# Performance work log

Measured on AMD Instinct MI355X. Metric: run time of the kernel, lower is better.

## Reference

```python
import jax, jax.numpy as jnp
import numpy as np
from functools import partial

U, I, D, E = 8192, 8192, 128, 524288
N = U + I


def setup_inputs() -> dict:
    key = jax.random.key(0)
    ks = jax.random.split(key, 12)
    s = 1.0 / np.sqrt(D)
    return {
        "user_emb": jax.random.normal(ks[0], (U, D), jnp.float32) * 0.1,
        "item_emb": jax.random.normal(ks[1], (I, D), jnp.float32) * 0.1,
        "adj_rows": jax.random.randint(ks[2], (E,), 0, N, jnp.int32),
        "adj_cols": jax.random.randint(ks[3], (E,), 0, N, jnp.int32),
        "adj_vals": jax.random.uniform(ks[4], (E,), jnp.float32) * (1.0 / 32.0),
        "wq": jax.random.normal(ks[5], (D, D), jnp.float32) * s,
        "bq": jnp.zeros((D,), jnp.float32),
        "wk": jax.random.normal(ks[6], (D, D), jnp.float32) * s,
        "bk": jnp.zeros((D,), jnp.float32),
        "wv": jax.random.normal(ks[7], (D, D), jnp.float32) * s,
        "bv": jnp.zeros((D,), jnp.float32),
        "fw": jax.random.normal(ks[8], (D, D), jnp.float32) * s,
        "fb": jnp.zeros((D,), jnp.float32),
        "n_layers": 3,
        "topk": 32,
    }


def _spmm(vals, rows, cols, x):
    # sparse [N,N] @ dense [N,D] via gather + segment_sum
    return jax.ops.segment_sum(vals[:, None] * x[cols], rows, num_segments=N)


def reference(user_emb, item_emb, adj_rows, adj_cols, adj_vals,
              wq, bq, wk, bk, wv, bv, fw, fb, n_layers, topk):
    ego = jnp.concatenate([user_emb, item_emb], axis=0)  # [N, D]
    layers = []
    for _ in range(n_layers):
        ego = _spmm(adj_vals, adj_rows, adj_cols, ego)
        layers.append(ego)
    all_emb = jnp.mean(jnp.stack(layers, axis=1), axis=1)  # [N, D]

    # full similarity + topk + gather
    sim = ego @ ego.T                                # [N, N]
    idx = jax.lax.top_k(sim, topk)[1]                # [N, K]
    samples = jnp.take(ego, idx, axis=0)             # [N, K, D]

    # per-node small attention over the K samples (dropout = eval identity)
    q = ego @ wq.T + bq                              # [N, D]
    k_ = samples @ wk.T + bk                         # [N, K, D]
    v = samples @ wv.T + bv                          # [N, K, D]
    scores = jnp.einsum('nd,nkd->nk', q, k_) / jnp.sqrt(jnp.float32(D))
    attn = jax.nn.softmax(scores, axis=-1)
    atten_embed = jnp.einsum('nk,nkd->nd', attn, v) + 0.1 * ego

    # fusion gating (softmax over dim=1, i.e. the node axis, as in source)
    a1 = jnp.tanh(all_emb @ fw.T + fb)
    a2 = jnp.tanh(atten_embed @ fw.T + fb)
    a = jax.nn.softmax(jnp.stack([a1, a2], axis=0), axis=1)  # [2, N, D]
    fusion = a[0] * all_emb + a[1] * atten_embed

    return (all_emb[:U], all_emb[U:],
            atten_embed[:U], atten_embed[U:],
            fusion[:U], fusion[U:])
```

## Files before the change

### kernel.cpp

```cpp
#include <hip/hip_runtime.h>
#include <math.h>

#define U_ 8192
#define I_ 8192
#define D_ 128
#define E_ 524288
#define N_ 16384
#define K_ 32
#define CAP_ 512

typedef unsigned short u16;
typedef unsigned int u32;
typedef unsigned long long u64;
typedef __attribute__((ext_vector_type(8))) short bf16x8;
typedef __attribute__((ext_vector_type(4))) float f32x4;

__global__ void k_init(const float* __restrict__ wq, const float* __restrict__ wk,
                       const float* __restrict__ bq, const float* __restrict__ wv,
                       const float* __restrict__ fw,
                       float* __restrict__ M, float* __restrict__ bqk,
                       float* __restrict__ wvT, float* __restrict__ fwdT,
                       int* __restrict__ cnt, float* __restrict__ cs1,
                       float* __restrict__ cs2,
                       float* __restrict__ svec, int* __restrict__ gcount,
                       int* __restrict__ failn) {
  const int tid = blockIdx.x * 256 + threadIdx.x;
  cnt[tid] = 0;
  gcount[tid] = 0;
  if (tid < 2048) { cs1[tid] = 0.f; cs2[tid] = 0.f; }
  if (tid < 128) svec[tid] = 0.f;
  if (tid == 0) *failn = 0;
  const int i = tid >> 7, j = tid & 127;
  float s = 0.f;
  for (int l = 0; l < 128; ++l) s += wq[l * 128 + i] * wk[l * 128 + j];
  M[tid] = s;
  wvT[i * 128 + j] = wv[j * 128 + i];
  fwdT[i * 128 + j] = fw[j * 128 + i];
  if (tid < 128) {
    float s2 = 0.f;
    for (int l = 0; l < 128; ++l) s2 += bq[l] * wk[l * 128 + tid];
    bqk[tid] = s2;
  }
}

__global__ void k_concat(const float* __restrict__ user, const float* __restrict__ item,
                         float* __restrict__ ego) {
  const int i = blockIdx.x * 256 + threadIdx.x;
  ego[i] = (i < U_ * D_) ? user[i] : item[i - U_ * D_];
}

__global__ void k_hist(const int* __restrict__ rows, int* __restrict__ cnt) {
  const int e = blockIdx.x * 256 + threadIdx.x;
  atomicAdd(&cnt[rows[e]], 1);
}

__global__ void k_scan(const int* __restrict__ cnt, int* __restrict__ row_ptr,
                       int* __restrict__ cursor) {
  __shared__ int wsum[16];
  __shared__ int carry_s;
  const int t = threadIdx.x;
  const int lane = t & 63, wid = t >> 6;
  if (t == 0) carry_s = 0;
  __syncthreads();
  for (int c = 0; c < N_ / 1024; ++c) {
    const int x = cnt[c * 1024 + t];
    int incl = x;
#pragma unroll
    for (int off = 1; off < 64; off <<= 1) {
      const int v = __shfl_up(incl, off, 64);
      if (lane >= off) incl += v;
    }
    if (lane == 63) wsum[wid] = incl;
    __syncthreads();
    if (wid == 0) {
      int s = (lane < 16) ? wsum[lane] : 0;
#pragma unroll
      for (int off = 1; off < 16; off <<= 1) {
        const int v = __shfl_up(s, off, 64);
        if (lane >= off) s += v;
      }
      if (lane < 16) wsum[lane] = s;
    }
    __syncthreads();
    const int carry = carry_s;
    const int wbase = wid ? wsum[wid - 1] : 0;
    const int excl = carry + wbase + incl - x;
    row_ptr[c * 1024 + t] = excl;
    cursor[c * 1024 + t] = excl;
    __syncthreads();
    if (t == 1023) carry_s += wsum[15];
    __syncthreads();
  }
  if (t == 0) row_ptr[N_] = carry_s;
}

__global__ void k_scatter(const int* __restrict__ rows, const int* __restrict__ cols,
                          const float* __restrict__ vals, int* __restrict__ cursor,
                          int* __restrict__ ccol, float* __restrict__ cval) {
  const int e = blockIdx.x * 256 + threadIdx.x;
  const int r = rows[e];
  const int p = atomicAdd(&cursor[r], 1);
  ccol[p] = cols[e];
  cval[p] = vals[e];
}

__global__ __launch_bounds__(128) void k_spmm(const float* __restrict__ x,
                                              float* __restrict__ y,
                                              float* __restrict__ sum,
                                              const int* __restrict__ row_ptr,
                                              const int* __restrict__ ccol,
                                              const float* __restrict__ cval,
                                              const int first) {
  const int r = blockIdx.x, d = threadIdx.x;
  const int b = row_ptr[r], e = row_ptr[r + 1];
  double acc = 0.0;
  for (int i = b; i < e; ++i)
    acc += (double)cval[i] * (double)x[ccol[i] * 128 + d];
  const float f = (float)acc;
  y[r * 128 + d] = f;
  if (first) sum[r * 128 + d] = f; else sum[r * 128 + d] += f;
}

__global__ void k_div3(float* __restrict__ a) {
  const int i = blockIdx.x * 256 + threadIdx.x;
  a[i] = a[i] / 3.0f;
}

__global__ __launch_bounds__(256) void k_split_t(const float* __restrict__ x,
                                                 u16* __restrict__ Gh, u16* __restrict__ Gl,
                                                 u16* __restrict__ XTh, u16* __restrict__ XTl,
                                                 float* __restrict__ svec) {
  __shared__ u16 lh[128 * 66];
  __shared__ u16 ll[128 * 66];
  const int tid = threadIdx.x;
  const int r0 = blockIdx.x * 64;
  float colsum = 0.f;
  for (int s = 0; s < 32; ++s) {
    const int idx = tid + s * 256;
    const int r = idx >> 7, d = idx & 127;
    const float v = x[(r0 + r) * 128 + d];
    colsum += v;
    unsigned int u = __float_as_uint(v);
    u += 0x7fffu + ((u >> 16) & 1u);
    const u16 h = (u16)(u >> 16);
    const float hf = __uint_as_float(((unsigned int)h) << 16);
    const float l = v - hf;
    unsigned int u2 = __float_as_uint(l);
    u2 += 0x7fffu + ((u2 >> 16) & 1u);
    const u16 lo = (u16)(u2 >> 16);
    Gh[(r0 + r) * 128 + d] = h;
    Gl[(r0 + r) * 128 + d] = lo;
    lh[d * 66 + r] = h;
    ll[d * 66 + r] = lo;
  }
  atomicAdd(&svec[tid & 127], colsum);
  __syncthreads();
  for (int s = 0; s < 32; ++s) {
    const int idx = tid + s * 256;
    const int d = idx >> 6, rr = idx & 63;
    XTh[d * 16384 + r0 + rr] = lh[d * 66 + rr];
    XTl[d * 16384 + r0 + rr] = ll[d * 66 + rr];
  }
}

__global__ __launch_bounds__(256) void k_c2mfma(const u16* __restrict__ XTh,
                                                const u16* __restrict__ XTl,
                                                float* __restrict__ C2part) {
  const int tid = threadIdx.x, w = tid >> 6, lane = tid & 63;
  const int n16 = lane & 15, kq = lane >> 4;
  const int c0 = blockIdx.x * 64;
  f32x4 acc[2][8];
#pragma unroll
  for (int a = 0; a < 2; ++a)
#pragma unroll
    for (int b = 0; b < 8; ++b) acc[a][b] = (f32x4){0.f, 0.f, 0.f, 0.f};
  for (int ks = 0; ks < 2; ++ks) {
    const int c = c0 + ks * 32 + kq * 8;
    bf16x8 Fh[8], Fl[8];
#pragma unroll
    for (int g = 0; g < 8; ++g) {
      const int base = (g * 16 + n16) * 16384 + c;
      Fh[g] = *(const bf16x8*)&XTh[base];
      Fl[g] = *(const bf16x8*)&XTl[base];
    }
#pragma unroll
    for (int a = 0; a < 2; ++a) {
      const int tr = w * 2 + a;
#pragma unroll
      for (int b = 0; b < 8; ++b) {
        acc[a][b] = __builtin_amdgcn_mfma_f32_16x16x32_bf16(Fl[tr], Fh[b], acc[a][b], 0, 0, 0);
        acc[a][b] = __builtin_amdgcn_mfma_f32_16x16x32_bf16(Fh[tr], Fl[b], acc[a][b], 0, 0, 0);
        acc[a][b] = __builtin_amdgcn_mfma_f32_16x16x32_bf16(Fh[tr], Fh[b], acc[a][b], 0, 0, 0);
      }
    }
  }
  float* dst = C2part + (size_t)blockIdx.x * 16384;
#pragma unroll
  for (int a = 0; a < 2; ++a) {
    const int tr = w * 2 + a;
#pragma unroll
    for (int b = 0; b < 8; ++b)
#pragma unroll
      for (int i = 0; i < 4; ++i)
        dst[(tr * 16 + kq * 4 + i) * 128 + b * 16 + n16] = acc[a][b][i];
  }
}

__global__ void k_c2red(const float* __restrict__ C2part, float* __restrict__ C2) {
  const int e = blockIdx.x * 256 + threadIdx.x;
  float s = 0.f;
  for (int b = 0; b < 256; ++b) s += C2part[(size_t)b * 16384 + e];
  C2[e] = s;
}

__global__ __launch_bounds__(128) void k_tau(const float* __restrict__ x,
                                             const float* __restrict__ C2,
                                             const float* __restrict__ svec,
                                             float* __restrict__ tau) {
  __shared__ float xs[128];
  __shared__ double red[128];
  const int n = blockIdx.x, tid = threadIdx.x;
  xs[tid] = x[n * 128 + tid];
  __syncthreads();
  double y = 0.0;
  for (int k2 = 0; k2 < 128; ++k2) y += (double)xs[k2] * (double)C2[k2 * 128 + tid];
  red[tid] = (double)xs[tid] * y;
  __syncthreads();
  for (int s = 64; s; s >>= 1) { if (tid < s) red[tid] += red[tid + s]; __syncthreads(); }
  const double exy = red[0] / 16384.0;
  __syncthreads();
  red[tid] = (double)xs[tid] * (double)svec[tid];
  __syncthreads();
  for (int s = 64; s; s >>= 1) { if (tid < s) red[tid] += red[tid + s]; __syncthreads(); }
  if (tid == 0) {
    const double m = red[0] / 16384.0;
    double var = exy - m * m;
    if (var < 0.0) var = 0.0;
    tau[n] = (float)(m + 2.55 * sqrt(var));
  }
}

__global__ __launch_bounds__(256) void k_qk(const float* __restrict__ ego,
                                            const float* __restrict__ M,
                                            const float* __restrict__ bqk,
                                            float* __restrict__ qkout) {
  __shared__ float xs[8][128];
  const int tid = threadIdx.x;
  const int r0 = blockIdx.x * 8;
#pragma unroll
  for (int s = 0; s < 4; ++s) {
    const int idx = tid + s * 256;
    xs[idx >> 7][idx & 127] = ego[r0 * 128 + idx];
  }
  __syncthreads();
  const int j = tid & 127, h = tid >> 7;
  const float bj = bqk[j];
  float acc[4];
#pragma unroll
  for (int r = 0; r < 4; ++r) acc[r] = bj;
  for (int d = 0; d < 128; d += 4) {
    const float w0 = M[(d + 0) * 128 + j];
    const float w1 = M[(d + 1) * 128 + j];
    const float w2 = M[(d + 2) * 128 + j];
    const float w3 = M[(d + 3) * 128 + j];
#pragma unroll
    for (int r = 0; r < 4; ++r) {
      const float4 xv = *(const float4*)&xs[h * 4 + r][d];
      acc[r] += xv.x * w0 + xv.y * w1 + xv.z * w2 + xv.w * w3;
    }
  }
#pragma unroll
  for (int r = 0; r < 4; ++r)
    qkout[(r0 + h * 4 + r) * 128 + j] = acc[r];
}

__device__ __forceinline__ void gload_lds16(const u16* g, u16* l) {
  __builtin_amdgcn_global_load_lds(
      (const __attribute__((address_space(1))) void*)g,
      (__attribute__((address_space(3))) void*)l, 16, 0, 0);
}

__global__ __launch_bounds__(256) void k_simmfma(const u16* __restrict__ Gh,
                                                 const u16* __restrict__ Gl,
                                                 const float* __restrict__ tau,
                                                 int* __restrict__ gstripcnt,
                                                 int2* __restrict__ gbuf) {
  __shared__ __align__(16) u16 lh[64 * 128];
  __shared__ int cnt128[128];
  const int tid = threadIdx.x;
  const int w = tid >> 6, lane = tid & 63;
  const int strip = blockIdx.x & 15, rgrp = blockIdx.x >> 4;
  const int n16 = lane & 15, kq = lane >> 4;

  if (tid < 128) cnt128[tid] = 0;

  const int rowbase = rgrp * 128 + w * 32;
  bf16x8 Bh[2][4], Bl[2][4];
#pragma unroll
  for (int rg = 0; rg < 2; ++rg) {
    const int row = rowbase + rg * 16 + n16;
#pragma unroll
    for (int q = 0; q < 4; ++q) {
      Bh[rg][q] = *(const bf16x8*)&Gh[row * 128 + q * 32 + kq * 8];
      Bl[rg][q] = *(const bf16x8*)&Gl[row * 128 + q * 32 + kq * 8];
    }
  }
  const float tau0 = tau[rowbase + n16];
  const float tau1 = tau[rowbase + 16 + n16];
  const int col0 = strip * 1024;

  for (int st = 0; st < 16; ++st) {
    const int cb = col0 + st * 64;
    __syncthreads();
#pragma unroll
    for (int ii = 0; ii < 4; ++ii) {
      const int srow = w * 16 + ii * 4 + kq;
      const int chunk = n16 ^ (srow & 7);
      gload_lds16(Gh + (((size_t)(cb + srow)) << 7) + chunk * 8,
                  lh + ((w * 16 + ii * 4) << 7));
    }
    __syncthreads();
#pragma unroll
    for (int ct = 0; ct < 4; ++ct) {
      const int ar = ct * 16 + n16;
      const char* lbase = (const char*)lh + ar * 256;
      bf16x8 Ah[4];
#pragma unroll
      for (int q = 0; q < 4; ++q)
        Ah[q] = *(const bf16x8*)(lbase + ((q * 64 + kq * 16) ^ ((ar & 7) << 4)));
#pragma unroll
      for (int rg = 0; rg < 2; ++rg) {
        f32x4 p = {0.f, 0.f, 0.f, 0.f};
        f32x4 r = {0.f, 0.f, 0.f, 0.f};
#pragma unroll
        for (int q = 0; q < 4; ++q) {
          p = __builtin_amdgcn_mfma_f32_16x16x32_bf16(Ah[q], Bh[rg][q], p, 0, 0, 0);
          r = __builtin_amdgcn_mfma_f32_16x16x32_bf16(Ah[q], Bl[rg][q], r, 0, 0, 0);
        }
        const float tv = rg ? tau1 : tau0;
        const int lrow = w * 32 + rg * 16 + n16;
        const int row = rgrp * 128 + lrow;
#pragma unroll
        for (int i = 0; i < 4; ++i) {
          const float v = p[i] + r[i];
          if (v > tv) {
            const int c = cb + ct * 16 + kq * 4 + i;
            const int pos = atomicAdd(&cnt128[lrow], 1);
            if (pos < 32)
              gbuf[row * CAP_ + strip * 32 + pos] = make_int2(c, __float_as_int(v));
          }
        }
      }
    }
  }
  __syncthreads();
  if (tid < 128) gstripcnt[(rgrp * 128 + tid) * 16 + strip] = cnt128[tid];
}

__global__ void k_check(const int* __restrict__ gstripcnt, int* __restrict__ failq,
                        int* __restrict__ failn) {
  const int n = blockIdx.x * 256 + threadIdx.x;
  int total = 0; int over = 0;
#pragma unroll
  for (int s = 0; s < 16; ++s) {
    const int c = gstripcnt[n * 16 + s];
    total += c;
    over |= (c > 32);
  }
  if (total < 36 || total > CAP_ || over) {
    const int s = atomicAdd(failn, 1);
    if (s < 64) failq[s] = n;
  }
}

__global__ __launch_bounds__(256) void k_refine(const int* __restrict__ gstripcnt,
                                                const int2* __restrict__ gbuf,
                                                int* __restrict__ topk_idx) {
  __shared__ u64 lk[4][CAP_];
  const int tid = threadIdx.x, w = tid >> 6, lane = tid & 63;
  const int n = blockIdx.x * 4 + w;

  const int scn = (lane < 16) ? gstripcnt[n * 16 + lane] : 0;
  int total = 0, over = 0;
#pragma unroll
  for (int s = 0; s < 16; ++s) {
    const int c = __shfl(scn, s, 64);
    total += c;
    over |= (c > 32);
  }
  const int bad = (total < 36 || total > CAP_ || over);
  const int cnt = bad ? 0 : total;

  int base = 0;
#pragma unroll
  for (int s = 0; s < 16; ++s) {
    const int c = __shfl(scn, s, 64);
    if (!bad && lane < c) {
      const int2 p = gbuf[n * CAP_ + s * 32 + lane];
      u32 uv = (u32)p.y;
      uv = (uv >> 31) ? ~uv : (uv | 0x80000000u);
      lk[w][base + lane] = ((u64)uv << 32) | (u64)(16383 - p.x);
    }
    base += bad ? 0 : c;
  }
  __syncthreads();

  for (int ci = lane; ci < cnt; ci += 64) {
    const u64 kk = lk[w][ci];
    int r = 0;
#pragma unroll 4
    for (int j = 0; j < cnt; ++j)
      r += (lk[w][j] > kk) ? 1 : 0;
    if (r < 32) topk_idx[n * 32 + r] = 16383 - (int)(u32)(kk & 0xffffffffu);
  }
  if (bad && lane < 32) topk_idx[n * 32 + lane] = 0;
}

__global__ __launch_bounds__(256) void k_fallback(const float* __restrict__ x,
                                                  const int* __restrict__ failq,
                                                  const int* __restrict__ failn,
                                                  double* __restrict__ fsim,
                                                  int* __restrict__ topk_idx) {
  const int nf = *failn;
  const int which = blockIdx.x;
  if (which >= nf || which >= 64) return;
  const int row = failq[which];
  __shared__ float xs[128];
  __shared__ double bm[256];
  __shared__ int bc[256];
  const int tid = threadIdx.x;
  if (tid < 128) xs[tid] = x[row * 128 + tid];
  __syncthreads();
  double* fs = fsim + (size_t)which * 16384;
  for (int c = tid; c < 16384; c += 256) {
    const float4* xp = (const float4*)&x[c * 128];
    double a = 0.0;
    for (int d = 0; d < 32; ++d) {
      const float4 v = xp[d];
      a += (double)xs[d * 4 + 0] * (double)v.x + (double)xs[d * 4 + 1] * (double)v.y +
           (double)xs[d * 4 + 2] * (double)v.z + (double)xs[d * 4 + 3] * (double)v.w;
    }
    fs[c] = a;
  }
  __syncthreads();
  for (int r = 0; r < 32; ++r) {
    double m = -1.0e300; int mc = 0;
    for (int c = tid; c < 16384; c += 256) {
      const double v = fs[c];
      if (v > m || (v == m && c < mc)) { m = v; mc = c; }
    }
    bm[tid] = m; bc[tid] = mc;
    __syncthreads();
    for (int s = 128; s; s >>= 1) {
      if (tid < s) {
        if (bm[tid + s] > bm[tid] || (bm[tid + s] == bm[tid] && bc[tid + s] < bc[tid])) {
          bm[tid] = bm[tid + s]; bc[tid] = bc[tid + s];
        }
      }
      __syncthreads();
    }
    if (tid == 0) { topk_idx[row * 32 + r] = bc[0]; fs[bc[0]] = -1.0e300; }
    __syncthreads();
  }
}

__global__ __launch_bounds__(128) void k_attn(const float* __restrict__ ego,
                                              const float* __restrict__ qk,
                                              const int* __restrict__ topk_idx,
                                              const float* __restrict__ wvT,
                                              const float* __restrict__ bv,
                                              float* __restrict__ atten) {
  __shared__ float qv[128];
  __shared__ float sm[32 * 129];
  __shared__ int tki[32];
  __shared__ float sc[32];
  __shared__ float sa[128];
  __shared__ float psum[128];
  const int n = blockIdx.x, tid = threadIdx.x;
  qv[tid] = qk[n * 128 + tid];
  if (tid < 32) tki[tid] = topk_idx[n * 32 + tid] & 16383;
  __syncthreads();
  for (int e = tid; e < 32 * 128; e += 128) {
    const int k2 = e >> 7, d = e & 127;
    sm[k2 * 129 + d] = ego[tki[k2] * 128 + d];
  }
  __syncthreads();
  {
    const int kk = tid & 31, part = tid >> 5;
    float s = 0.f;
    const int d0 = part * 32;
    for (int d = d0; d < d0 + 32; ++d) s += qv[d] * sm[kk * 129 + d];
    psum[tid] = s;
  }
  __syncthreads();
  if (tid < 32) {
    float v = psum[tid] + psum[tid + 32] + psum[tid + 64] + psum[tid + 96];
    v *= (1.0f / 11.313708498984760f);
    float m = v;
#pragma unroll
    for (int off = 16; off; off >>= 1) m = fmaxf(m, __shfl_xor(m, off, 32));
    const float e = expf(v - m);
    float ssum = e;
#pragma unroll
    for (int off = 16; off; off >>= 1) ssum += __shfl_xor(ssum, off, 32);
    sc[tid] = e / ssum;
  }
  __syncthreads();
  float sad = 0.f;
  for (int k2 = 0; k2 < 32; ++k2) sad += sc[k2] * sm[k2 * 129 + tid];
  sa[tid] = sad;
  __syncthreads();
  float o = bv[tid];
  for (int d = 0; d < 128; ++d) o += sa[d] * wvT[d * 128 + tid];
  atten[n * 128 + tid] = o + 0.1f * ego[n * 128 + tid];
}

__global__ __launch_bounds__(256) void k_fuse1(const float* __restrict__ allemb,
                                               const float* __restrict__ atten,
                                               const float* __restrict__ fwdT,
                                               const float* __restrict__ fb,
                                               float* __restrict__ z1,
                                               float* __restrict__ z2,
                                               float* __restrict__ cs1,
                                               float* __restrict__ cs2) {
  __shared__ float xs[8][128];
  __shared__ float as[8][128];
  __shared__ float red1[2][128];
  __shared__ float red2[2][128];
  const int tid = threadIdx.x;
  const int r0 = blockIdx.x * 8;
#pragma unroll
  for (int s = 0; s < 4; ++s) {
    const int idx = tid + s * 256;
    const int rr = idx >> 7, d = idx & 127;
    xs[rr][d] = allemb[(r0 + rr) * 128 + d];
    as[rr][d] = atten[(r0 + rr) * 128 + d];
  }
  __syncthreads();
  const int j = tid & 127, h = tid >> 7;
  const float fbj = fb[j];
  float acc1[4], acc2[4];
#pragma unroll
  for (int r = 0; r < 4; ++r) { acc1[r] = fbj; acc2[r] = fbj; }
  for (int d = 0; d < 128; d += 4) {
    const float w0 = fwdT[(d + 0) * 128 + j];
    const float w1 = fwdT[(d + 1) * 128 + j];
    const float w2 = fwdT[(d + 2) * 128 + j];
    const float w3 = fwdT[(d + 3) * 128 + j];
#pragma unroll
    for (int r = 0; r < 4; ++r) {
      const int rr = h * 4 + r;
      const float4 xv = *(const float4*)&xs[rr][d];
      const float4 av = *(const float4*)&as[rr][d];
      acc1[r] += xv.x * w0 + xv.y * w1 + xv.z * w2 + xv.w * w3;
      acc2[r] += av.x * w0 + av.y * w1 + av.z * w2 + av.w * w3;
    }
  }
  float ls1 = 0.f, ls2 = 0.f;
#pragma unroll
  for (int r = 0; r < 4; ++r) {
    const int rr = h * 4 + r;
    const float t1 = tanhf(acc1[r]);
    const float t2 = tanhf(acc2[r]);
    z1[(r0 + rr) * 128 + j] = t1;
    z2[(r0 + rr) * 128 + j] = t2;
    ls1 += expf(t1 - 1.0f);
    ls2 += expf(t2 - 1.0f);
  }
  red1[h][j] = ls1;
  red2[h][j] = ls2;
  __syncthreads();
  if (h == 0) {
    const int rep = blockIdx.x & 15;
    atomicAdd(&cs1[rep * 128 + j], red1[0][j] + red1[1][j]);
    atomicAdd(&cs2[rep * 128 + j], red2[0][j] + red2[1][j]);
  }
}

__global__ void k_fuse2(const float* __restrict__ allemb, const float* __restrict__ atten,
                        const float* __restrict__ z1, const float* __restrict__ z2,
                        const float* __restrict__ cs1, const float* __restrict__ cs2,
                        float* __restrict__ fusion) {
  __shared__ float s1[128], s2[128];
  const int tid = threadIdx.x;
  if (tid < 128) {
    float a = 0.f, b = 0.f;
#pragma unroll
    for (int rep = 0; rep < 16; ++rep) {
      a += cs1[rep * 128 + tid];
      b += cs2[rep * 128 + tid];
    }
    s1[tid] = a; s2[tid] = b;
  }
  __syncthreads();
  const int i = blockIdx.x * 256 + tid;
  const int j = i & 127;
  const float a1 = expf(z1[i] - 1.0f) / s1[j];
  const float a2 = expf(z2[i] - 1.0f) / s2[j];
  fusion[i] = a1 * allemb[i] + a2 * atten[i];
}

extern "C" void kernel_launch(void* const* d_in, const int* in_sizes, int n_in,
                              void* d_out, int out_size, void* d_ws, size_t ws_size,
                              hipStream_t stream) {
  (void)in_sizes; (void)n_in; (void)out_size; (void)ws_size;
  const float* user = (const float*)d_in[0];
  const float* item = (const float*)d_in[1];
  const int* adj_rows = (const int*)d_in[2];
  const int* adj_cols = (const int*)d_in[3];
  const float* adj_vals = (const float*)d_in[4];
  const float* wq = (const float*)d_in[5];
  const float* bq = (const float*)d_in[6];
  const float* wk = (const float*)d_in[7];
  const float* wv = (const float*)d_in[9];
  const float* bv = (const float*)d_in[10];
  const float* fw = (const float*)d_in[11];
  const float* fb = (const float*)d_in[12];

  float* out = (float*)d_out;
  float* allemb = out;
  float* atten = out + (size_t)N_ * D_;
  float* fusion = out + (size_t)2 * N_ * D_;

  char* ws = (char*)d_ws;
  size_t off = 0;
  auto alloc = [&](size_t bytes) { char* p = ws + off; off += (bytes + 255) & ~(size_t)255; return p; };
  float* ego_a = (float*)alloc((size_t)N_ * D_ * 4);
  float* ego_b = (float*)alloc((size_t)N_ * D_ * 4);
  float* qkbuf = (float*)alloc((size_t)N_ * D_ * 4);
  u16* Gh = (u16*)alloc((size_t)N_ * D_ * 2);
  u16* Gl = (u16*)alloc((size_t)N_ * D_ * 2);
  u16* XTh = (u16*)alloc((size_t)N_ * D_ * 2);
  u16* XTl = (u16*)alloc((size_t)N_ * D_ * 2);
  int2* gbuf = (int2*)alloc((size_t)N_ * CAP_ * 8);
  float* z1 = (float*)gbuf;
  float* z2 = (float*)alloc((size_t)N_ * D_ * 4);
  int* topk_idx = (int*)alloc((size_t)N_ * 32 * 4);
  int* ccol = (int*)alloc((size_t)E_ * 4);
  float* cval = (float*)alloc((size_t)E_ * 4);
  int* cnt = (int*)alloc((size_t)N_ * 4);
  int* row_ptr = (int*)alloc((size_t)(N_ + 1) * 4);
  int* cursor = (int*)alloc((size_t)N_ * 4);
  float* M = (float*)alloc(128 * 128 * 4);
  float* bqk = (float*)alloc(128 * 4);
  float* wvT = (float*)alloc(128 * 128 * 4);
  float* fwdT = (float*)alloc(128 * 128 * 4);
  float* cs1 = (float*)alloc(16 * 128 * 4);
  float* cs2 = (float*)alloc(16 * 128 * 4);
  float* C2 = (float*)alloc(128 * 128 * 4);
  float* C2part = (float*)alloc((size_t)256 * 16384 * 4);
  float* svec = (float*)alloc(128 * 4);
  float* tau = (float*)alloc((size_t)N_ * 4);
  int* gcount = (int*)alloc((size_t)N_ * 4);
  int* gstripcnt = (int*)alloc((size_t)N_ * 16 * 4);
  int* failq = (int*)alloc(64 * 4);
  int* failn = (int*)alloc(4);
  double* fsim = (double*)alloc((size_t)64 * N_ * 8);

  k_init<<<64, 256, 0, stream>>>(wq, wk, bq, wv, fw, M, bqk, wvT, fwdT, cnt, cs1, cs2, svec, gcount, failn);
  k_concat<<<8192, 256, 0, stream>>>(user, item, ego_a);
  k_hist<<<2048, 256, 0, stream>>>(adj_rows, cnt);
  k_scan<<<1, 1024, 0, stream>>>(cnt, row_ptr, cursor);
  k_scatter<<<2048, 256, 0, stream>>>(adj_rows, adj_cols, adj_vals, cursor, ccol, cval);

  k_spmm<<<N_, 128, 0, stream>>>(ego_a, ego_b, allemb, row_ptr, ccol, cval, 1);
  k_spmm<<<N_, 128, 0, stream>>>(ego_b, ego_a, allemb, row_ptr, ccol, cval, 0);
  k_spmm<<<N_, 128, 0, stream>>>(ego_a, ego_b, allemb, row_ptr, ccol, cval, 0);
  k_div3<<<8192, 256, 0, stream>>>(allemb);

  k_split_t<<<256, 256, 0, stream>>>(ego_b, Gh, Gl, XTh, XTl, svec);
  k_c2mfma<<<256, 256, 0, stream>>>(XTh, XTl, C2part);
  k_c2red<<<64, 256, 0, stream>>>(C2part, C2);
  k_tau<<<N_, 128, 0, stream>>>(ego_b, C2, svec, tau);

  k_qk<<<2048, 256, 0, stream>>>(ego_b, M, bqk, qkbuf);
  k_simmfma<<<2048, 256, 0, stream>>>(Gh, Gl, tau, gstripcnt, gbuf);
  k_check<<<64, 256, 0, stream>>>(gstripcnt, failq, failn);
  k_refine<<<4096, 256, 0, stream>>>(gstripcnt, gbuf, topk_idx);
  k_fallback<<<64, 256, 0, stream>>>(ego_b, failq, failn, fsim, topk_idx);
  k_attn<<<N_, 128, 0, stream>>>(ego_b, qkbuf, topk_idx, wvT, bv, atten);

  k_fuse1<<<2048, 256, 0, stream>>>(allemb, atten, fwdT, fb, z1, z2, cs1, cs2);
  k_fuse2<<<8192, 256, 0, stream>>>(allemb, atten, z1, z2, cs1, cs2, fusion);
}
```

Before: 787.0 us.

## Fuse div3 into last SpMM, batch tau rows, split attention value projection

Folds the divide-by-three into the final SpMM launch and drops the separate k_div3 pass. The SpMM inner loop gets four independent double accumulators, which changes the summation order slightly. k_tau now handles 8 rows per block so C2 is read once per 8 rows instead of once per row. The value-projection matmul moves out of the per-node attention kernel into a batched 8-row kernel that reuses wvT across rows, with qkbuf reused as the intermediate buffer at the cost of one extra launch.

```diff
diff --git a/kernel.cpp b/kernel.cpp
--- a/kernel.cpp
+++ b/kernel.cpp
@@ -110,20 +110,24 @@
                                               const int* __restrict__ row_ptr,
                                               const int* __restrict__ ccol,
                                               const float* __restrict__ cval,
-                                              const int first) {
+                                              const int first, const int last) {
   const int r = blockIdx.x, d = threadIdx.x;
   const int b = row_ptr[r], e = row_ptr[r + 1];
-  double acc = 0.0;
-  for (int i = b; i < e; ++i)
-    acc += (double)cval[i] * (double)x[ccol[i] * 128 + d];
-  const float f = (float)acc;
+  double a0 = 0.0, a1 = 0.0, a2 = 0.0, a3 = 0.0;
+  int i = b;
+  for (; i + 3 < e; i += 4) {
+    a0 += (double)cval[i + 0] * (double)x[ccol[i + 0] * 128 + d];
+    a1 += (double)cval[i + 1] * (double)x[ccol[i + 1] * 128 + d];
+    a2 += (double)cval[i + 2] * (double)x[ccol[i + 2] * 128 + d];
+    a3 += (double)cval[i + 3] * (double)x[ccol[i + 3] * 128 + d];
+  }
+  for (; i < e; ++i)
+    a0 += (double)cval[i] * (double)x[ccol[i] * 128 + d];
+  const float f = (float)((a0 + a1) + (a2 + a3));
   y[r * 128 + d] = f;
-  if (first) sum[r * 128 + d] = f; else sum[r * 128 + d] += f;
-}
-
-__global__ void k_div3(float* __restrict__ a) {
-  const int i = blockIdx.x * 256 + threadIdx.x;
-  a[i] = a[i] / 3.0f;
+  float s = first ? f : sum[r * 128 + d] + f;
+  if (last) s = s / 3.0f;
+  sum[r * 128 + d] = s;
 }
 
 __global__ __launch_bounds__(256) void k_split_t(const float* __restrict__ x,
@@ -217,26 +221,38 @@
                                              const float* __restrict__ C2,
                                              const float* __restrict__ svec,
                                              float* __restrict__ tau) {
-  __shared__ float xs[128];
+  __shared__ float xs[8][128];
   __shared__ double red[128];
-  const int n = blockIdx.x, tid = threadIdx.x;
-  xs[tid] = x[n * 128 + tid];
-  __syncthreads();
-  double y = 0.0;
-  for (int k2 = 0; k2 < 128; ++k2) y += (double)xs[k2] * (double)C2[k2 * 128 + tid];
-  red[tid] = (double)xs[tid] * y;
-  __syncthreads();
-  for (int s = 64; s; s >>= 1) { if (tid < s) red[tid] += red[tid + s]; __syncthreads(); }
-  const double exy = red[0] / 16384.0;
-  __syncthreads();
-  red[tid] = (double)xs[tid] * (double)svec[tid];
-  __syncthreads();
-  for (int s = 64; s; s >>= 1) { if (tid < s) red[tid] += red[tid + s]; __syncthreads(); }
-  if (tid == 0) {
-    const double m = red[0] / 16384.0;
-    double var = exy - m * m;
-    if (var < 0.0) var = 0.0;
-    tau[n] = (float)(m + 2.55 * sqrt(var));
+  const int tid = threadIdx.x;
+  const int n0 = blockIdx.x * 8;
+#pragma unroll
+  for (int rr = 0; rr < 8; ++rr) xs[rr][tid] = x[(n0 + rr) * 128 + tid];
+  __syncthreads();
+  double y[8];
+#pragma unroll
+  for (int rr = 0; rr < 8; ++rr) y[rr] = 0.0;
+  for (int k2 = 0; k2 < 128; ++k2) {
+    const double c = (double)C2[k2 * 128 + tid];
+#pragma unroll
+    for (int rr = 0; rr < 8; ++rr) y[rr] += (double)xs[rr][k2] * c;
+  }
+  const double sv = (double)svec[tid];
+  for (int rr = 0; rr < 8; ++rr) {
+    red[tid] = (double)xs[rr][tid] * y[rr];
+    __syncthreads();
+    for (int s = 64; s; s >>= 1) { if (tid < s) red[tid] += red[tid + s]; __syncthreads(); }
+    const double exy = red[0] / 16384.0;
+    __syncthreads();
+    red[tid] = (double)xs[rr][tid] * sv;
+    __syncthreads();
+    for (int s = 64; s; s >>= 1) { if (tid < s) red[tid] += red[tid + s]; __syncthreads(); }
+    if (tid == 0) {
+      const double m = red[0] / 16384.0;
+      double var = exy - m * m;
+      if (var < 0.0) var = 0.0;
+      tau[n0 + rr] = (float)(m + 2.55 * sqrt(var));
+    }
+    __syncthreads();
   }
 }
 
@@ -465,16 +481,12 @@
 }
 
 __global__ __launch_bounds__(128) void k_attn(const float* __restrict__ ego,
-                                              const float* __restrict__ qk,
-                                              const int* __restrict__ topk_idx,
-                                              const float* __restrict__ wvT,
-                                              const float* __restrict__ bv,
-                                              float* __restrict__ atten) {
+                                              float* __restrict__ qk,
+                                              const int* __restrict__ topk_idx) {
   __shared__ float qv[128];
   __shared__ float sm[32 * 129];
   __shared__ int tki[32];
   __shared__ float sc[32];
-  __shared__ float sa[128];
   __shared__ float psum[128];
   const int n = blockIdx.x, tid = threadIdx.x;
   qv[tid] = qk[n * 128 + tid];
@@ -508,11 +520,44 @@
   __syncthreads();
   float sad = 0.f;
   for (int k2 = 0; k2 < 32; ++k2) sad += sc[k2] * sm[k2 * 129 + tid];
-  sa[tid] = sad;
-  __syncthreads();
-  float o = bv[tid];
-  for (int d = 0; d < 128; ++d) o += sa[d] * wvT[d * 128 + tid];
-  atten[n * 128 + tid] = o + 0.1f * ego[n * 128 + tid];
+  qk[n * 128 + tid] = sad;
+}
+
+__global__ __launch_bounds__(256) void k_attnmm(const float* __restrict__ sa,
+                                                const float* __restrict__ ego,
+                                                const float* __restrict__ wvT,
+                                                const float* __restrict__ bv,
+                                                float* __restrict__ atten) {
+  __shared__ float xs[8][128];
+  const int tid = threadIdx.x;
+  const int r0 = blockIdx.x * 8;
+#pragma unroll
+  for (int s = 0; s < 4; ++s) {
+    const int idx = tid + s * 256;
+    xs[idx >> 7][idx & 127] = sa[r0 * 128 + idx];
+  }
+  __syncthreads();
+  const int j = tid & 127, h = tid >> 7;
+  const float bj = bv[j];
+  float acc[4];
+#pragma unroll
+  for (int r = 0; r < 4; ++r) acc[r] = bj;
+  for (int d = 0; d < 128; d += 4) {
+    const float w0 = wvT[(d + 0) * 128 + j];
+    const float w1 = wvT[(d + 1) * 128 + j];
+    const float w2 = wvT[(d + 2) * 128 + j];
+    const float w3 = wvT[(d + 3) * 128 + j];
+#pragma unroll
+    for (int r = 0; r < 4; ++r) {
+      const float4 xv = *(const float4*)&xs[h * 4 + r][d];
+      acc[r] += xv.x * w0 + xv.y * w1 + xv.z * w2 + xv.w * w3;
+    }
+  }
+#pragma unroll
+  for (int r = 0; r < 4; ++r) {
+    const int n = r0 + h * 4 + r;
+    atten[n * 128 + j] = acc[r] + 0.1f * ego[n * 128 + j];
+  }
 }
 
 __global__ __launch_bounds__(256) void k_fuse1(const float* __restrict__ allemb,
@@ -663,22 +708,22 @@
   k_scan<<<1, 1024, 0, stream>>>(cnt, row_ptr, cursor);
   k_scatter<<<2048, 256, 0, stream>>>(adj_rows, adj_cols, adj_vals, cursor, ccol, cval);
 
-  k_spmm<<<N_, 128, 0, stream>>>(ego_a, ego_b, allemb, row_ptr, ccol, cval, 1);
-  k_spmm<<<N_, 128, 0, stream>>>(ego_b, ego_a, allemb, row_ptr, ccol, cval, 0);
-  k_spmm<<<N_, 128, 0, stream>>>(ego_a, ego_b, allemb, row_ptr, ccol, cval, 0);
-  k_div3<<<8192, 256, 0, stream>>>(allemb);
+  k_spmm<<<N_, 128, 0, stream>>>(ego_a, ego_b, allemb, row_ptr, ccol, cval, 1, 0);
+  k_spmm<<<N_, 128, 0, stream>>>(ego_b, ego_a, allemb, row_ptr, ccol, cval, 0, 0);
+  k_spmm<<<N_, 128, 0, stream>>>(ego_a, ego_b, allemb, row_ptr, ccol, cval, 0, 1);
 
   k_split_t<<<256, 256, 0, stream>>>(ego_b, Gh, Gl, XTh, XTl, svec);
   k_c2mfma<<<256, 256, 0, stream>>>(XTh, XTl, C2part);
   k_c2red<<<64, 256, 0, stream>>>(C2part, C2);
-  k_tau<<<N_, 128, 0, stream>>>(ego_b, C2, svec, tau);
+  k_tau<<<2048, 128, 0, stream>>>(ego_b, C2, svec, tau);
 
   k_qk<<<2048, 256, 0, stream>>>(ego_b, M, bqk, qkbuf);
   k_simmfma<<<2048, 256, 0, stream>>>(Gh, Gl, tau, gstripcnt, gbuf);
   k_check<<<64, 256, 0, stream>>>(gstripcnt, failq, failn);
   k_refine<<<4096, 256, 0, stream>>>(gstripcnt, gbuf, topk_idx);
   k_fallback<<<64, 256, 0, stream>>>(ego_b, failq, failn, fsim, topk_idx);
-  k_attn<<<N_, 128, 0, stream>>>(ego_b, qkbuf, topk_idx, wvT, bv, atten);
+  k_attn<<<N_, 128, 0, stream>>>(ego_b, qkbuf, topk_idx);
+  k_attnmm<<<2048, 256, 0, stream>>>(qkbuf, ego_b, wvT, bv, atten);
 
   k_fuse1<<<2048, 256, 0, stream>>>(allemb, atten, fwdT, fb, z1, z2, cs1, cs2);
   k_fuse2<<<8192, 256, 0, stream>>>(allemb, atten, z1, z2, cs1, cs2, fusion);
```

New measurement: 687.1 us. 12.7% less time.
